# Optimization experiments

Hardware: AMD Instinct MI355X
Metric: run time of the kernel (lower is better)

The kernel has to match this reference:

```python
import jax, jax.numpy as jnp
import numpy as np

D_MODEL = 256
D_INNER = 512   # expand=2
D_STATE = 16
DT_RANK = 16    # ceil(d_model/16)
D_CONV = 4
N_LAYERS = 2    # per direction
B, N = 2, 1024


def _mamba_layer(x, W_in, cw, cb, W_x, W_dt, b_dt, A_log, Dp, W_out):
    """One mamba_ssm.Mamba forward. x: (B, L, d_model)."""
    Bb, L, _ = x.shape
    xz = x @ W_in.T                        # (B, L, 2*d_inner)
    di = xz.shape[-1] // 2
    xc, z = xz[..., :di], xz[..., di:]
    # causal depthwise conv1d, kernel D_CONV, left-pad d_conv-1
    K = cw.shape[-1]
    xp = jnp.pad(xc, ((0, 0), (K - 1, 0), (0, 0)))
    xc = sum(xp[:, k:k + L, :] * cw[:, k] for k in range(K)) + cb
    xc = jax.nn.silu(xc)
    # input-dependent dt, B, C
    dbl = xc @ W_x.T                       # (B, L, dt_rank + 2*d_state)
    ds = A_log.shape[-1]
    dt = dbl[..., :DT_RANK]
    Bm = dbl[..., DT_RANK:DT_RANK + ds]    # (B, L, d_state)
    Cm = dbl[..., DT_RANK + ds:]           # (B, L, d_state)
    dt = jax.nn.softplus(dt @ W_dt.T + b_dt)  # (B, L, d_inner)
    A = -jnp.exp(A_log)                    # (d_inner, d_state)
    dA = jnp.exp(dt[..., None] * A)                          # (B, L, di, ds)
    dBx = dt[..., None] * Bm[:, :, None, :] * xc[..., None]  # (B, L, di, ds)

    def step(h, inp):
        a_t, b_t, c_t = inp                # (B,di,ds),(B,di,ds),(B,ds)
        h = a_t * h + b_t
        y_t = jnp.einsum('bds,bs->bd', h, c_t)
        return h, y_t

    h0 = jnp.zeros((Bb, di, ds), x.dtype)
    _, ys = jax.lax.scan(step, h0, (dA.transpose(1, 0, 2, 3),
                                    dBx.transpose(1, 0, 2, 3),
                                    Cm.transpose(1, 0, 2)))
    y = ys.transpose(1, 0, 2) + xc * Dp    # skip term D*x
    y = y * jax.nn.silu(z)                 # gate
    return y @ W_out.T                     # (B, L, d_model)


def setup_inputs() -> dict:
    key = jax.random.key(0)
    ks = jax.random.split(key, 10)
    s = 0.05  # weight scale for numerical stability
    nlay = 2 * N_LAYERS  # forward layers then backward layers
    return {
        "x": jax.random.normal(ks[0], (B, N, D_MODEL), jnp.float32),
        "in_proj": jax.random.normal(ks[1], (nlay, 2 * D_INNER, D_MODEL), jnp.float32) * s,
        "conv_w": jax.random.normal(ks[2], (nlay, D_INNER, D_CONV), jnp.float32) * s,
        "conv_b": jax.random.normal(ks[3], (nlay, D_INNER), jnp.float32) * s,
        "x_proj": jax.random.normal(ks[4], (nlay, DT_RANK + 2 * D_STATE, D_INNER), jnp.float32) * s,
        "dt_proj": jax.random.normal(ks[5], (nlay, D_INNER, DT_RANK), jnp.float32) * s,
        "dt_bias": jax.random.normal(ks[6], (nlay, D_INNER), jnp.float32) * s,
        "A_log": jax.random.uniform(ks[7], (nlay, D_INNER, D_STATE), jnp.float32),
        "D": jax.random.uniform(ks[8], (nlay, D_INNER), jnp.float32),
        "out_proj": jax.random.normal(ks[9], (nlay, D_MODEL, D_INNER), jnp.float32) * s,
    }


def reference(x, in_proj, conv_w, conv_b, x_proj, dt_proj, dt_bias, A_log, D, out_proj):
    n = in_proj.shape[0] // 2
    x_fwd = x
    for i in range(n):
        x_fwd = _mamba_layer(x_fwd, in_proj[i], conv_w[i], conv_b[i], x_proj[i],
                             dt_proj[i], dt_bias[i], A_log[i], D[i], out_proj[i])
    x_bwd = x[:, ::-1, :]
    for i in range(n, 2 * n):
        x_bwd = _mamba_layer(x_bwd, in_proj[i], conv_w[i], conv_b[i], x_proj[i],
                             dt_proj[i], dt_bias[i], A_log[i], D[i], out_proj[i])
    x_bwd = x_bwd[:, ::-1, :]
    return jnp.concatenate([x_fwd, x_bwd], axis=-1)  # (B, N, 2*d_model)
```

## Files before the change

kernel.cpp:

```cpp
#include <hip/hip_runtime.h>
#include <math.h>

#define G 2
#define BB 2
#define L 1024
#define DM 256
#define DI 512
#define DS 16
#define DR 16
#define CH 64
#define CL 16
#define RTOT (G*BB*L)
#define YSTR 520
#define XSTR 520

#define NWIN  (4 * 2 * DI * DM)
#define NWOUT (4 * DM * DI)
#define NWX   (4 * 48 * DI)

typedef short bh8 __attribute__((ext_vector_type(8)));
typedef float f4x __attribute__((ext_vector_type(4)));

__device__ __forceinline__ float silu_f(float x) { return x / (1.f + __expf(-x)); }
__device__ __forceinline__ float softplus_f(float x) {
    return (x > 20.f) ? x : __logf(1.f + __expf(x));
}

__device__ __forceinline__ unsigned short f2bf(float f) {
    unsigned u = __float_as_uint(f);
    unsigned r = u + 0x7FFFu + ((u >> 16) & 1u);
    return (unsigned short)(r >> 16);
}
__device__ __forceinline__ float bf2f(unsigned short s) {
    return __uint_as_float(((unsigned)s) << 16);
}

__global__ __launch_bounds__(256) void cvtW3(
    const float* __restrict__ Wa, short* __restrict__ Wah, short* __restrict__ Wal, int n4a,
    const float* __restrict__ Wb, short* __restrict__ Wbh, short* __restrict__ Wbl, int n4b,
    const float* __restrict__ Wc, short* __restrict__ Wch, short* __restrict__ Wcl, int n4c)
{
    int i = blockIdx.x * 256 + threadIdx.x;
    const float* W; short *Wh, *Wl;
    if (i < n4a) { W = Wa; Wh = Wah; Wl = Wal; }
    else if (i < n4a + n4b) { i -= n4a; W = Wb; Wh = Wbh; Wl = Wbl; }
    else if (i < n4a + n4b + n4c) { i -= n4a + n4b; W = Wc; Wh = Wch; Wl = Wcl; }
    else return;
    float4 v = *(const float4*)&W[(size_t)i * 4];
    short4 h, l;
    unsigned short s;
    s = f2bf(v.x); h.x = (short)s; l.x = (short)f2bf(v.x - bf2f(s));
    s = f2bf(v.y); h.y = (short)s; l.y = (short)f2bf(v.y - bf2f(s));
    s = f2bf(v.z); h.z = (short)s; l.z = (short)f2bf(v.z - bf2f(s));
    s = f2bf(v.w); h.w = (short)s; l.w = (short)f2bf(v.w - bf2f(s));
    *(short4*)&Wh[(size_t)i * 4] = h;
    *(short4*)&Wl[(size_t)i * 4] = l;
}

template<int AMAP>
__global__ __launch_bounds__(256) void mfma_inproj(
    const float* __restrict__ Ax,
    const short* __restrict__ Ah, const short* __restrict__ Al,
    const short* __restrict__ Wh, const short* __restrict__ Wl,
    int step, float* __restrict__ C)
{
    constexpr int BM = 128, Ktot = DM, Nout = 2 * DI, ldc = 1024;
    __shared__ short As_hi[BM * 40];
    __shared__ short As_lo[BM * 40];
    __shared__ short Bs_hi[64 * 40];
    __shared__ short Bs_lo[64 * 40];

    const int row0 = blockIdx.y * BM;
    const int col0 = blockIdx.x * 64;
    const int g    = row0 >> 11;
    const int lay  = g * 2 + step;
    const short* Whg = Wh + (size_t)lay * Nout * Ktot;
    const short* Wlg = Wl + (size_t)lay * Nout * Ktot;
    const int t    = threadIdx.x;
    const int lane = t & 63, wv = t >> 6;
    const int m = lane & 15, quad = lane >> 4;
    const int wr = wv >> 1, wc = wv & 1;
    const int NT = Ktot / 32;

    float4 pa[4];
    short4 pah[4], pal[4], pbh[2], pbl[2];
    auto loadT = [&](int kt) {
        const int kb = kt * 32;
        #pragma unroll
        for (int i = 0; i < 4; i++) {
            int id = t + 256 * i;
            int row = id >> 3, kq = id & 7;
            if (AMAP == 1) {
                int gr = row0 + row;
                int gg = gr >> 11, b = (gr >> 10) & 1, l = gr & 1023;
                int sl = gg ? (1023 - l) : l;
                pa[i] = *(const float4*)&Ax[(size_t)(b * 1024 + sl) * Ktot + kb + kq * 4];
            } else {
                size_t o = (size_t)(row0 + row) * Ktot + kb + kq * 4;
                pah[i] = *(const short4*)&Ah[o];
                pal[i] = *(const short4*)&Al[o];
            }
        }
        #pragma unroll
        for (int i = 0; i < 2; i++) {
            int id = t + 256 * i;
            int row = id >> 3, kq = id & 7;
            size_t o = (size_t)(col0 + row) * Ktot + kb + kq * 4;
            pbh[i] = *(const short4*)&Whg[o];
            pbl[i] = *(const short4*)&Wlg[o];
        }
    };

    f4x acc[4][2] = {};
    loadT(0);

    for (int kt = 0; kt < NT; kt++) {
        #pragma unroll
        for (int i = 0; i < 4; i++) {
            int id = t + 256 * i;
            int row = id >> 3, kq = id & 7;
            if (AMAP == 1) {
                float4 v = pa[i];
                short4 h, l;
                unsigned short s;
                s = f2bf(v.x); h.x = (short)s; l.x = (short)f2bf(v.x - bf2f(s));
                s = f2bf(v.y); h.y = (short)s; l.y = (short)f2bf(v.y - bf2f(s));
                s = f2bf(v.z); h.z = (short)s; l.z = (short)f2bf(v.z - bf2f(s));
                s = f2bf(v.w); h.w = (short)s; l.w = (short)f2bf(v.w - bf2f(s));
                *(short4*)&As_hi[row * 40 + kq * 4] = h;
                *(short4*)&As_lo[row * 40 + kq * 4] = l;
            } else {
                *(short4*)&As_hi[row * 40 + kq * 4] = pah[i];
                *(short4*)&As_lo[row * 40 + kq * 4] = pal[i];
            }
        }
        #pragma unroll
        for (int i = 0; i < 2; i++) {
            int id = t + 256 * i;
            int row = id >> 3, kq = id & 7;
            *(short4*)&Bs_hi[row * 40 + kq * 4] = pbh[i];
            *(short4*)&Bs_lo[row * 40 + kq * 4] = pbl[i];
        }
        __syncthreads();
        if (kt + 1 < NT) loadT(kt + 1);

        bh8 ah[4], al[4], bh[2], bl[2];
        #pragma unroll
        for (int p = 0; p < 4; p++) {
            int r = wr * 64 + p * 16 + m;
            ah[p] = *(bh8*)&As_hi[r * 40 + quad * 8];
            al[p] = *(bh8*)&As_lo[r * 40 + quad * 8];
        }
        #pragma unroll
        for (int q = 0; q < 2; q++) {
            int r = wc * 32 + q * 16 + m;
            bh[q] = *(bh8*)&Bs_hi[r * 40 + quad * 8];
            bl[q] = *(bh8*)&Bs_lo[r * 40 + quad * 8];
        }
        #pragma unroll
        for (int p = 0; p < 4; p++)
            #pragma unroll
            for (int q = 0; q < 2; q++) {
                acc[p][q] = __builtin_amdgcn_mfma_f32_16x16x32_bf16(ah[p], bh[q], acc[p][q], 0, 0, 0);
                acc[p][q] = __builtin_amdgcn_mfma_f32_16x16x32_bf16(ah[p], bl[q], acc[p][q], 0, 0, 0);
                acc[p][q] = __builtin_amdgcn_mfma_f32_16x16x32_bf16(al[p], bh[q], acc[p][q], 0, 0, 0);
            }
        __syncthreads();
    }

    #pragma unroll
    for (int p = 0; p < 4; p++)
        #pragma unroll
        for (int q = 0; q < 2; q++) {
            int gcol = col0 + wc * 32 + q * 16 + m;
            #pragma unroll
            for (int r = 0; r < 4; r++) {
                int grow = row0 + wr * 64 + p * 16 + quad * 4 + r;
                C[(size_t)grow * ldc + gcol] = acc[p][q][r];
            }
        }
}

__global__ __launch_bounds__(512) void scanA2(
    const float* __restrict__ XZ, const float* __restrict__ cw,
    const float* __restrict__ cb,
    const short* __restrict__ Wxh, const short* __restrict__ Wxl,
    const float* __restrict__ A_log, const float* __restrict__ Wdt,
    const float* __restrict__ bdt,
    float* __restrict__ XCb, float* __restrict__ DBLc,
    float* __restrict__ Aprod, float* __restrict__ Hend, int step)
{
    __shared__ short xcH[CL * XSTR];
    __shared__ short xcL[CL * XSTR];
    __shared__ float part[8][CL][48];
    __shared__ float dbl[CL][48];

    const int blk = blockIdx.x;
    const int c  = blk & (CH - 1);
    const int gb = blk >> 6;
    const int g  = gb >> 1;
    const int lay = g * 2 + step;
    const int d  = threadIdx.x;
    const int r0 = gb * L + c * CL;

    float4 w4 = *(const float4*)&cw[((size_t)lay * DI + d) * 4];
    float cbv = cb[(size_t)lay * DI + d];
    float xz[CL + 3];
    #pragma unroll
    for (int j = 0; j < CL + 3; j++) {
        int lr = c * CL + j - 3;
        xz[j] = (lr < 0) ? 0.f : XZ[(size_t)(gb * L + lr) * 1024 + d];
    }
    float xc[CL];
    #pragma unroll
    for (int tt = 0; tt < CL; tt++) {
        float v = cbv + w4.x * xz[tt] + w4.y * xz[tt + 1]
                      + w4.z * xz[tt + 2] + w4.w * xz[tt + 3];
        v = silu_f(v);
        xc[tt] = v;
        XCb[(size_t)(r0 + tt) * DI + d] = v;
        unsigned short hs = f2bf(v);
        xcH[tt * XSTR + d] = (short)hs;
        xcL[tt * XSTR + d] = (short)f2bf(v - bf2f(hs));
    }
    __syncthreads();

    {
        const int lane = d & 63, wv = d >> 6;
        const int m = lane & 15, quad = lane >> 4;
        const int ks = wv * 64;
        const size_t wb = (size_t)lay * 48 * DI;
        f4x acc[3] = {};
        #pragma unroll
        for (int kt = 0; kt < 2; kt++) {
            const int kb = ks + kt * 32 + quad * 8;
            bh8 ah = *(bh8*)&xcH[m * XSTR + kb];
            bh8 al = *(bh8*)&xcL[m * XSTR + kb];
            #pragma unroll
            for (int f = 0; f < 3; f++) {
                bh8 bh = *(const bh8*)&Wxh[wb + (size_t)(f * 16 + m) * DI + kb];
                bh8 bl = *(const bh8*)&Wxl[wb + (size_t)(f * 16 + m) * DI + kb];
                acc[f] = __builtin_amdgcn_mfma_f32_16x16x32_bf16(ah, bh, acc[f], 0, 0, 0);
                acc[f] = __builtin_amdgcn_mfma_f32_16x16x32_bf16(ah, bl, acc[f], 0, 0, 0);
                acc[f] = __builtin_amdgcn_mfma_f32_16x16x32_bf16(al, bh, acc[f], 0, 0, 0);
            }
        }
        #pragma unroll
        for (int f = 0; f < 3; f++)
            #pragma unroll
            for (int r = 0; r < 4; r++)
                part[wv][quad * 4 + r][f * 16 + m] = acc[f][r];
    }
    __syncthreads();

    for (int o = d; o < CL * 48; o += 512) {
        int tt = o / 48, cc = o - tt * 48;
        float v = 0.f;
        #pragma unroll
        for (int w = 0; w < 8; w++) v += part[w][tt][cc];
        dbl[tt][cc] = v;
        DBLc[(size_t)(r0 + tt) * 48 + cc] = v;
    }

    float wdt[16];
    const float* wrow = Wdt + ((size_t)lay * DI + d) * DR;
    #pragma unroll
    for (int k = 0; k < 16; k += 4) {
        float4 v = *(const float4*)&wrow[k];
        wdt[k] = v.x; wdt[k + 1] = v.y; wdt[k + 2] = v.z; wdt[k + 3] = v.w;
    }
    float bias = bdt[(size_t)lay * DI + d];

    float a[DS], h[DS], ap[DS];
    const float* al = A_log + ((size_t)lay * DI + d) * DS;
    #pragma unroll
    for (int s = 0; s < DS; s++) { a[s] = -__expf(al[s]); h[s] = 0.f; ap[s] = 1.f; }
    __syncthreads();

    for (int tt = 0; tt < CL; tt++) {
        float dtr = bias;
        #pragma unroll
        for (int k = 0; k < 16; k++) dtr += dbl[tt][k] * wdt[k];
        float dt = softplus_f(dtr);
        float dx = dt * xc[tt];
        #pragma unroll
        for (int s = 0; s < DS; s++) {
            float da = __expf(dt * a[s]);
            h[s] = da * h[s] + dx * dbl[tt][16 + s];
            ap[s] *= da;
        }
    }
    size_t base = ((size_t)(gb * DI + d) * CH + c) * DS;
    #pragma unroll
    for (int q = 0; q < 4; q++) {
        *(float4*)&Aprod[base + q * 4] = make_float4(ap[q*4], ap[q*4+1], ap[q*4+2], ap[q*4+3]);
        *(float4*)&Hend [base + q * 4] = make_float4(h[q*4],  h[q*4+1],  h[q*4+2],  h[q*4+3]);
    }
}

__global__ __launch_bounds__(256) void scanCombine(
    const float* __restrict__ Aprod, const float* __restrict__ Hend,
    float* __restrict__ Hinit)
{
    int idx = blockIdx.x * 256 + threadIdx.x;
    int s  = idx & 15;
    int gd = idx >> 4;
    size_t base = (size_t)gd * CH * DS + s;
    float h = 0.f;
    for (int c0 = 0; c0 < CH; c0 += 8) {
        float ap[8], e[8];
        #pragma unroll
        for (int j = 0; j < 8; j++) {
            size_t o = base + (size_t)(c0 + j) * DS;
            ap[j] = Aprod[o]; e[j] = Hend[o];
        }
        #pragma unroll
        for (int j = 0; j < 8; j++) {
            Hinit[base + (size_t)(c0 + j) * DS] = h;
            h = ap[j] * h + e[j];
        }
    }
}

template<int OUTMODE>
__global__ __launch_bounds__(512) void scanB_fused(
    const float* __restrict__ XCb, const float* __restrict__ DBLc,
    const float* __restrict__ XZ, const float* __restrict__ A_log,
    const float* __restrict__ Wdt, const float* __restrict__ bdt,
    const float* __restrict__ Dp, const float* __restrict__ Hinit,
    const short* __restrict__ Woh, const short* __restrict__ Wol,
    float* __restrict__ Cout, short* __restrict__ Ph, short* __restrict__ Pl,
    int step)
{
    __shared__ float dbl[CL][48];
    __shared__ short Ys_hi[CL * YSTR];
    __shared__ short Ys_lo[CL * YSTR];
    int blk = blockIdx.x;
    int c  = blk & (CH - 1);
    int gb = blk >> 6;
    int g  = gb >> 1;
    int lay = g * 2 + step;
    int d = threadIdx.x;
    int r0 = gb * L + c * CL;

    for (int id = threadIdx.x; id < CL * 48; id += 512) {
        int rr = id / 48, cc = id - rr * 48;
        dbl[rr][cc] = DBLc[(size_t)(r0 + rr) * 48 + cc];
    }

    float xc[CL], zz[CL];
    #pragma unroll
    for (int tt = 0; tt < CL; tt++) xc[tt] = XCb[(size_t)(r0 + tt) * DI + d];
    #pragma unroll
    for (int tt = 0; tt < CL; tt++) zz[tt] = XZ[(size_t)(r0 + tt) * 1024 + 512 + d];

    float wdt[16];
    const float* wrow = Wdt + ((size_t)lay * DI + d) * DR;
    #pragma unroll
    for (int k = 0; k < 16; k += 4) {
        float4 v = *(const float4*)&wrow[k];
        wdt[k] = v.x; wdt[k + 1] = v.y; wdt[k + 2] = v.z; wdt[k + 3] = v.w;
    }
    float bias = bdt[(size_t)lay * DI + d];

    float a[DS], h[DS];
    const float* al = A_log + ((size_t)lay * DI + d) * DS;
    size_t base = ((size_t)(gb * DI + d) * CH + c) * DS;
    #pragma unroll
    for (int q = 0; q < 4; q++) {
        float4 hv = *(const float4*)&Hinit[base + q * 4];
        h[q*4] = hv.x; h[q*4+1] = hv.y; h[q*4+2] = hv.z; h[q*4+3] = hv.w;
    }
    #pragma unroll
    for (int s = 0; s < DS; s++) a[s] = -__expf(al[s]);
    float Dv = Dp[(size_t)lay * DI + d];
    __syncthreads();

    #pragma unroll
    for (int tt = 0; tt < CL; tt++) {
        float dtr = bias;
        #pragma unroll
        for (int k = 0; k < 16; k++) dtr += dbl[tt][k] * wdt[k];
        float dt = softplus_f(dtr);
        float dx = dt * xc[tt];
        float y = 0.f;
        #pragma unroll
        for (int s = 0; s < DS; s++) {
            float da = __expf(dt * a[s]);
            h[s] = da * h[s] + dx * dbl[tt][16 + s];
            y += h[s] * dbl[tt][32 + s];
        }
        y += xc[tt] * Dv;
        y *= silu_f(zz[tt]);
        unsigned short hs = f2bf(y);
        Ys_hi[tt * YSTR + d] = (short)hs;
        Ys_lo[tt * YSTR + d] = (short)f2bf(y - bf2f(hs));
    }
    __syncthreads();

    const int lane = threadIdx.x & 63, wv = threadIdx.x >> 6;
    const int m = lane & 15, quad = lane >> 4;
    const size_t wbase = (size_t)lay * DM * DI;

    #pragma unroll
    for (int q = 0; q < 2; q++) {
        const int coln = wv * 32 + q * 16 + m;
        const size_t wrow2 = wbase + (size_t)coln * DI;
        bh8 wh[16], wl[16];
        #pragma unroll
        for (int i = 0; i < 16; i++) {
            const int kk = i * 32 + quad * 8;
            wh[i] = *(const bh8*)&Woh[wrow2 + kk];
            wl[i] = *(const bh8*)&Wol[wrow2 + kk];
        }
        f4x acc = {};
        #pragma unroll
        for (int i = 0; i < 16; i++) {
            const int kk = i * 32 + quad * 8;
            bh8 ahv = *(bh8*)&Ys_hi[m * YSTR + kk];
            bh8 alv = *(bh8*)&Ys_lo[m * YSTR + kk];
            acc = __builtin_amdgcn_mfma_f32_16x16x32_bf16(ahv, wh[i], acc, 0, 0, 0);
            acc = __builtin_amdgcn_mfma_f32_16x16x32_bf16(ahv, wl[i], acc, 0, 0, 0);
            acc = __builtin_amdgcn_mfma_f32_16x16x32_bf16(alv, wh[i], acc, 0, 0, 0);
        }
        #pragma unroll
        for (int r = 0; r < 4; r++) {
            int tt = quad * 4 + r;
            int grow = r0 + tt;
            if (OUTMODE == 0) {
                size_t o = (size_t)grow * DM + coln;
                unsigned short hs = f2bf(acc[r]);
                Ph[o] = (short)hs;
                Pl[o] = (short)f2bf(acc[r] - bf2f(hs));
            } else {
                int b = (grow >> 10) & 1, l = grow & 1023;
                size_t dst = (g == 0)
                    ? ((size_t)(b * 1024 + l) * 512 + coln)
                    : ((size_t)(b * 1024 + (1023 - l)) * 512 + 256 + coln);
                Cout[dst] = acc[r];
            }
        }
    }
}

extern "C" void kernel_launch(void* const* d_in, const int* in_sizes, int n_in,
                              void* d_out, int out_size, void* d_ws, size_t ws_size,
                              hipStream_t stream)
{
    const float* x        = (const float*)d_in[0];
    const float* in_proj  = (const float*)d_in[1];
    const float* conv_w   = (const float*)d_in[2];
    const float* conv_b   = (const float*)d_in[3];
    const float* x_proj   = (const float*)d_in[4];
    const float* dt_proj  = (const float*)d_in[5];
    const float* dt_bias  = (const float*)d_in[6];
    const float* A_log    = (const float*)d_in[7];
    const float* Dp       = (const float*)d_in[8];
    const float* out_proj = (const float*)d_in[9];
    float* out = (float*)d_out;

    float* w = (float*)d_ws;
    size_t o = 0;
    float* XZ    = w + o; o += (size_t)RTOT * 1024;
    float* XCb   = w + o; o += (size_t)RTOT * DI;
    float* Pdbl  = w + o; o += (size_t)8 * RTOT * 48;
    float* DBLc  = w + o; o += (size_t)RTOT * 48;
    float* Aprod = w + o; o += (size_t)G * BB * DI * CH * DS;
    float* Hend  = w + o; o += (size_t)G * BB * DI * CH * DS;
    float* Hinit = w + o; o += (size_t)G * BB * DI * CH * DS;
    short* Wih   = (short*)(w + o); o += NWIN / 2;
    short* Wil   = (short*)(w + o); o += NWIN / 2;
    short* Woh   = (short*)(w + o); o += NWOUT / 2;
    short* Wol   = (short*)(w + o); o += NWOUT / 2;
    short* Ph    = (short*)(w + o); o += (size_t)RTOT * DM / 2;
    short* Pl    = (short*)(w + o); o += (size_t)RTOT * DM / 2;
    short* Wxh   = (short*)Pdbl;
    short* Wxl   = Wxh + NWX;
    (void)ws_size; (void)in_sizes; (void)n_in; (void)out_size;

    {
        int n4a = NWIN / 4, n4b = NWOUT / 4, n4c = NWX / 4;
        cvtW3<<<(n4a + n4b + n4c + 255) / 256, 256, 0, stream>>>(
            in_proj, Wih, Wil, n4a, out_proj, Woh, Wol, n4b,
            x_proj, Wxh, Wxl, n4c);
    }

    for (int step = 0; step < 2; step++) {
        if (step == 0)
            mfma_inproj<1><<<dim3(16, 32), 256, 0, stream>>>(
                x, nullptr, nullptr, Wih, Wil, 0, XZ);
        else
            mfma_inproj<0><<<dim3(16, 32), 256, 0, stream>>>(
                nullptr, Ph, Pl, Wih, Wil, 1, XZ);

        scanA2<<<G * BB * CH, 512, 0, stream>>>(
            XZ, conv_w, conv_b, Wxh, Wxl, A_log, dt_proj, dt_bias,
            XCb, DBLc, Aprod, Hend, step);

        scanCombine<<<(G * BB * DI * DS) / 256, 256, 0, stream>>>(Aprod, Hend, Hinit);

        if (step == 0)
            scanB_fused<0><<<G * BB * CH, 512, 0, stream>>>(
                XCb, DBLc, XZ, A_log, dt_proj, dt_bias, Dp, Hinit,
                Woh, Wol, nullptr, Ph, Pl, 0);
        else
            scanB_fused<1><<<G * BB * CH, 512, 0, stream>>>(
                XCb, DBLc, XZ, A_log, dt_proj, dt_bias, Dp, Hinit,
                Woh, Wol, out, nullptr, nullptr, 1);
    }
}
```

Baseline: 223.6 us.

## Fuse in_proj GEMM into scan-A kernel and split weights on the fly

Removes the separate in_proj GEMM kernel and fuses it into the per-chunk scan kernel. Each 16-row chunk block recomputes its own xz tile, including a 3-row halo for the causal conv, and keeps the conv input in shared memory, writing only z to global. The weight pre-conversion kernel is dropped: in_proj, x_proj and out_proj are read as fp32 and split into bf16 hi/lo pairs inside the MFMA loops. This saves two launches and the full XZ round trip through global memory. In exchange each block redoes weight loads and splits, the halo rows add extra GEMM work, and the in_proj GEMM now runs with a small M tile that gets little weight reuse.

```diff
diff --git a/kernel.cpp b/kernel.cpp
--- a/kernel.cpp
+++ b/kernel.cpp
@@ -14,12 +14,10 @@
 #define YSTR 520
 #define XSTR 520
 
-#define NWIN  (4 * 2 * DI * DM)
-#define NWOUT (4 * DM * DI)
-#define NWX   (4 * 48 * DI)
-
 typedef short bh8 __attribute__((ext_vector_type(8)));
 typedef float f4x __attribute__((ext_vector_type(4)));
+
+#define MFMA16 __builtin_amdgcn_mfma_f32_16x16x32_bf16
 
 __device__ __forceinline__ float silu_f(float x) { return x / (1.f + __expf(-x)); }
 __device__ __forceinline__ float softplus_f(float x) {
@@ -34,188 +32,142 @@
 __device__ __forceinline__ float bf2f(unsigned short s) {
     return __uint_as_float(((unsigned)s) << 16);
 }
-
-__global__ __launch_bounds__(256) void cvtW3(
-    const float* __restrict__ Wa, short* __restrict__ Wah, short* __restrict__ Wal, int n4a,
-    const float* __restrict__ Wb, short* __restrict__ Wbh, short* __restrict__ Wbl, int n4b,
-    const float* __restrict__ Wc, short* __restrict__ Wch, short* __restrict__ Wcl, int n4c)
-{
-    int i = blockIdx.x * 256 + threadIdx.x;
-    const float* W; short *Wh, *Wl;
-    if (i < n4a) { W = Wa; Wh = Wah; Wl = Wal; }
-    else if (i < n4a + n4b) { i -= n4a; W = Wb; Wh = Wbh; Wl = Wbl; }
-    else if (i < n4a + n4b + n4c) { i -= n4a + n4b; W = Wc; Wh = Wch; Wl = Wcl; }
-    else return;
-    float4 v = *(const float4*)&W[(size_t)i * 4];
-    short4 h, l;
+__device__ __forceinline__ void split4s(float4 v, short4& h, short4& l) {
     unsigned short s;
     s = f2bf(v.x); h.x = (short)s; l.x = (short)f2bf(v.x - bf2f(s));
     s = f2bf(v.y); h.y = (short)s; l.y = (short)f2bf(v.y - bf2f(s));
     s = f2bf(v.z); h.z = (short)s; l.z = (short)f2bf(v.z - bf2f(s));
     s = f2bf(v.w); h.w = (short)s; l.w = (short)f2bf(v.w - bf2f(s));
-    *(short4*)&Wh[(size_t)i * 4] = h;
-    *(short4*)&Wl[(size_t)i * 4] = l;
+}
+__device__ __forceinline__ void split8(float4 v0, float4 v1, bh8& h, bh8& l) {
+    float f[8] = {v0.x, v0.y, v0.z, v0.w, v1.x, v1.y, v1.z, v1.w};
+    #pragma unroll
+    for (int j = 0; j < 8; j++) {
+        unsigned short s = f2bf(f[j]);
+        h[j] = (short)s;
+        l[j] = (short)f2bf(f[j] - bf2f(s));
+    }
 }
 
 template<int AMAP>
-__global__ __launch_bounds__(256) void mfma_inproj(
+__global__ __launch_bounds__(512) void megaA(
     const float* __restrict__ Ax,
-    const short* __restrict__ Ah, const short* __restrict__ Al,
-    const short* __restrict__ Wh, const short* __restrict__ Wl,
-    int step, float* __restrict__ C)
-{
-    constexpr int BM = 128, Ktot = DM, Nout = 2 * DI, ldc = 1024;
-    __shared__ short As_hi[BM * 40];
-    __shared__ short As_lo[BM * 40];
-    __shared__ short Bs_hi[64 * 40];
-    __shared__ short Bs_lo[64 * 40];
-
-    const int row0 = blockIdx.y * BM;
-    const int col0 = blockIdx.x * 64;
-    const int g    = row0 >> 11;
-    const int lay  = g * 2 + step;
-    const short* Whg = Wh + (size_t)lay * Nout * Ktot;
-    const short* Wlg = Wl + (size_t)lay * Nout * Ktot;
-    const int t    = threadIdx.x;
-    const int lane = t & 63, wv = t >> 6;
-    const int m = lane & 15, quad = lane >> 4;
-    const int wr = wv >> 1, wc = wv & 1;
-    const int NT = Ktot / 32;
-
-    float4 pa[4];
-    short4 pah[4], pal[4], pbh[2], pbl[2];
-    auto loadT = [&](int kt) {
-        const int kb = kt * 32;
-        #pragma unroll
-        for (int i = 0; i < 4; i++) {
-            int id = t + 256 * i;
-            int row = id >> 3, kq = id & 7;
-            if (AMAP == 1) {
-                int gr = row0 + row;
-                int gg = gr >> 11, b = (gr >> 10) & 1, l = gr & 1023;
-                int sl = gg ? (1023 - l) : l;
-                pa[i] = *(const float4*)&Ax[(size_t)(b * 1024 + sl) * Ktot + kb + kq * 4];
-            } else {
-                size_t o = (size_t)(row0 + row) * Ktot + kb + kq * 4;
-                pah[i] = *(const short4*)&Ah[o];
-                pal[i] = *(const short4*)&Al[o];
-            }
-        }
-        #pragma unroll
-        for (int i = 0; i < 2; i++) {
-            int id = t + 256 * i;
-            int row = id >> 3, kq = id & 7;
-            size_t o = (size_t)(col0 + row) * Ktot + kb + kq * 4;
-            pbh[i] = *(const short4*)&Whg[o];
-            pbl[i] = *(const short4*)&Wlg[o];
-        }
-    };
-
-    f4x acc[4][2] = {};
-    loadT(0);
-
-    for (int kt = 0; kt < NT; kt++) {
-        #pragma unroll
-        for (int i = 0; i < 4; i++) {
-            int id = t + 256 * i;
-            int row = id >> 3, kq = id & 7;
-            if (AMAP == 1) {
-                float4 v = pa[i];
-                short4 h, l;
-                unsigned short s;
-                s = f2bf(v.x); h.x = (short)s; l.x = (short)f2bf(v.x - bf2f(s));
-                s = f2bf(v.y); h.y = (short)s; l.y = (short)f2bf(v.y - bf2f(s));
-                s = f2bf(v.z); h.z = (short)s; l.z = (short)f2bf(v.z - bf2f(s));
-                s = f2bf(v.w); h.w = (short)s; l.w = (short)f2bf(v.w - bf2f(s));
-                *(short4*)&As_hi[row * 40 + kq * 4] = h;
-                *(short4*)&As_lo[row * 40 + kq * 4] = l;
-            } else {
-                *(short4*)&As_hi[row * 40 + kq * 4] = pah[i];
-                *(short4*)&As_lo[row * 40 + kq * 4] = pal[i];
-            }
-        }
-        #pragma unroll
-        for (int i = 0; i < 2; i++) {
-            int id = t + 256 * i;
-            int row = id >> 3, kq = id & 7;
-            *(short4*)&Bs_hi[row * 40 + kq * 4] = pbh[i];
-            *(short4*)&Bs_lo[row * 40 + kq * 4] = pbl[i];
-        }
-        __syncthreads();
-        if (kt + 1 < NT) loadT(kt + 1);
-
-        bh8 ah[4], al[4], bh[2], bl[2];
-        #pragma unroll
-        for (int p = 0; p < 4; p++) {
-            int r = wr * 64 + p * 16 + m;
-            ah[p] = *(bh8*)&As_hi[r * 40 + quad * 8];
-            al[p] = *(bh8*)&As_lo[r * 40 + quad * 8];
-        }
-        #pragma unroll
-        for (int q = 0; q < 2; q++) {
-            int r = wc * 32 + q * 16 + m;
-            bh[q] = *(bh8*)&Bs_hi[r * 40 + quad * 8];
-            bl[q] = *(bh8*)&Bs_lo[r * 40 + quad * 8];
-        }
-        #pragma unroll
-        for (int p = 0; p < 4; p++)
-            #pragma unroll
-            for (int q = 0; q < 2; q++) {
-                acc[p][q] = __builtin_amdgcn_mfma_f32_16x16x32_bf16(ah[p], bh[q], acc[p][q], 0, 0, 0);
-                acc[p][q] = __builtin_amdgcn_mfma_f32_16x16x32_bf16(ah[p], bl[q], acc[p][q], 0, 0, 0);
-                acc[p][q] = __builtin_amdgcn_mfma_f32_16x16x32_bf16(al[p], bh[q], acc[p][q], 0, 0, 0);
-            }
-        __syncthreads();
-    }
-
-    #pragma unroll
-    for (int p = 0; p < 4; p++)
-        #pragma unroll
-        for (int q = 0; q < 2; q++) {
-            int gcol = col0 + wc * 32 + q * 16 + m;
-            #pragma unroll
-            for (int r = 0; r < 4; r++) {
-                int grow = row0 + wr * 64 + p * 16 + quad * 4 + r;
-                C[(size_t)grow * ldc + gcol] = acc[p][q][r];
-            }
-        }
-}
-
-__global__ __launch_bounds__(512) void scanA2(
-    const float* __restrict__ XZ, const float* __restrict__ cw,
-    const float* __restrict__ cb,
-    const short* __restrict__ Wxh, const short* __restrict__ Wxl,
+    const short* __restrict__ APh, const short* __restrict__ APl,
+    const float* __restrict__ Win, const float* __restrict__ cw,
+    const float* __restrict__ cb, const float* __restrict__ Wx,
     const float* __restrict__ A_log, const float* __restrict__ Wdt,
     const float* __restrict__ bdt,
-    float* __restrict__ XCb, float* __restrict__ DBLc,
+    float* __restrict__ XCb, float* __restrict__ Zb, float* __restrict__ DBLc,
     float* __restrict__ Aprod, float* __restrict__ Hend, int step)
 {
-    __shared__ short xcH[CL * XSTR];
-    __shared__ short xcL[CL * XSTR];
-    __shared__ float part[8][CL][48];
-    __shared__ float dbl[CL][48];
+    __shared__ __align__(16) char smem[73008];
+    short* Ah  = (short*)smem;
+    short* Al  = (short*)(smem + 16896);
+    float* xz  = (float*)(smem + 33792);
+    short* xcH = (short*)smem;
+    short* xcL = (short*)(smem + 16640);
+    float* part = (float*)(smem + 33792);
+    float* dbl  = (float*)(smem + 58368);
 
     const int blk = blockIdx.x;
-    const int c  = blk & (CH - 1);
-    const int gb = blk >> 6;
-    const int g  = gb >> 1;
+    const int c   = blk & (CH - 1);
+    const int gb  = blk >> 6;
+    const int g   = gb >> 1;
     const int lay = g * 2 + step;
-    const int d  = threadIdx.x;
-    const int r0 = gb * L + c * CL;
-
+    const int tid = threadIdx.x;
+    const int r0  = gb * L + c * CL;
+    const int lane = tid & 63, wv = tid >> 6;
+    const int m = lane & 15, quad = lane >> 4;
+
+    #pragma unroll
+    for (int i = 0; i < 4; i++) {
+        int id = tid + 512 * i;
+        int row = id >> 6, kq = id & 63;
+        int gr  = r0 - 16 + row;
+        int grc = (gr < gb * L) ? gb * L : gr;
+        if (AMAP == 1) {
+            int b = (grc >> 10) & 1, l = grc & 1023;
+            int sl = g ? (1023 - l) : l;
+            float4 v = *(const float4*)&Ax[(size_t)(b * 1024 + sl) * DM + kq * 4];
+            short4 h4, l4; split4s(v, h4, l4);
+            *(short4*)&Ah[row * 264 + kq * 4] = h4;
+            *(short4*)&Al[row * 264 + kq * 4] = l4;
+        } else {
+            size_t o = (size_t)grc * DM + kq * 4;
+            *(short4*)&Ah[row * 264 + kq * 4] = *(const short4*)&APh[o];
+            *(short4*)&Al[row * 264 + kq * 4] = *(const short4*)&APl[o];
+        }
+    }
+    __syncthreads();
+
+    const float* Wg = Win + (size_t)lay * 1024 * DM;
+    #pragma unroll
+    for (int ct = 0; ct < 2; ct++) {
+        const int colb = ct * 512 + wv * 64;
+        const int mt0 = ct;
+        f4x acc[2][4] = {};
+        for (int kt = 0; kt < 8; kt++) {
+            const int kb = kt * 32 + quad * 8;
+            bh8 ahf[2], alf[2];
+            #pragma unroll
+            for (int mt = 0; mt < 2; mt++) {
+                if (mt < mt0) continue;
+                ahf[mt] = *(bh8*)&Ah[(mt * 16 + m) * 264 + kb];
+                alf[mt] = *(bh8*)&Al[(mt * 16 + m) * 264 + kb];
+            }
+            float4 braw[4][2];
+            #pragma unroll
+            for (int nt = 0; nt < 4; nt++) {
+                const float* bp = &Wg[(size_t)(colb + nt * 16 + m) * DM + kb];
+                braw[nt][0] = *(const float4*)bp;
+                braw[nt][1] = *(const float4*)(bp + 4);
+            }
+            #pragma unroll
+            for (int nt = 0; nt < 4; nt++) {
+                bh8 bh, bl; split8(braw[nt][0], braw[nt][1], bh, bl);
+                #pragma unroll
+                for (int mt = 0; mt < 2; mt++) {
+                    if (mt < mt0) continue;
+                    acc[mt][nt] = MFMA16(ahf[mt], bh, acc[mt][nt], 0, 0, 0);
+                    acc[mt][nt] = MFMA16(ahf[mt], bl, acc[mt][nt], 0, 0, 0);
+                    acc[mt][nt] = MFMA16(alf[mt], bh, acc[mt][nt], 0, 0, 0);
+                }
+            }
+        }
+        #pragma unroll
+        for (int nt = 0; nt < 4; nt++) {
+            int gcol = colb + nt * 16 + m;
+            #pragma unroll
+            for (int mt = 0; mt < 2; mt++) {
+                if (mt < mt0) continue;
+                #pragma unroll
+                for (int r = 0; r < 4; r++) {
+                    int i = mt * 16 + quad * 4 + r;
+                    float v = acc[mt][nt][r];
+                    if (ct == 0) {
+                        if (i >= 13) xz[(i - 13) * 516 + gcol] = v;
+                    } else {
+                        if (i >= 16)
+                            Zb[(size_t)(r0 + i - 16) * 512 + (gcol - 512)] = v;
+                    }
+                }
+            }
+        }
+    }
+    __syncthreads();
+
+    const int d = tid;
     float4 w4 = *(const float4*)&cw[((size_t)lay * DI + d) * 4];
     float cbv = cb[(size_t)lay * DI + d];
-    float xz[CL + 3];
-    #pragma unroll
-    for (int j = 0; j < CL + 3; j++) {
-        int lr = c * CL + j - 3;
-        xz[j] = (lr < 0) ? 0.f : XZ[(size_t)(gb * L + lr) * 1024 + d];
-    }
+    float xzv[CL + 3];
+    #pragma unroll
+    for (int j = 0; j < CL + 3; j++)
+        xzv[j] = (c * CL + j - 3 < 0) ? 0.f : xz[j * 516 + d];
     float xc[CL];
     #pragma unroll
     for (int tt = 0; tt < CL; tt++) {
-        float v = cbv + w4.x * xz[tt] + w4.y * xz[tt + 1]
-                      + w4.z * xz[tt + 2] + w4.w * xz[tt + 3];
+        float v = cbv + w4.x * xzv[tt] + w4.y * xzv[tt + 1]
+                      + w4.z * xzv[tt + 2] + w4.w * xzv[tt + 3];
         v = silu_f(v);
         xc[tt] = v;
         XCb[(size_t)(r0 + tt) * DI + d] = v;
@@ -226,11 +178,9 @@
     __syncthreads();
 
     {
-        const int lane = d & 63, wv = d >> 6;
-        const int m = lane & 15, quad = lane >> 4;
         const int ks = wv * 64;
-        const size_t wb = (size_t)lay * 48 * DI;
-        f4x acc[3] = {};
+        const float* Wxg = Wx + (size_t)lay * 48 * DI;
+        f4x acc3[3] = {};
         #pragma unroll
         for (int kt = 0; kt < 2; kt++) {
             const int kb = ks + kt * 32 + quad * 8;
@@ -238,18 +188,19 @@
             bh8 al = *(bh8*)&xcL[m * XSTR + kb];
             #pragma unroll
             for (int f = 0; f < 3; f++) {
-                bh8 bh = *(const bh8*)&Wxh[wb + (size_t)(f * 16 + m) * DI + kb];
-                bh8 bl = *(const bh8*)&Wxl[wb + (size_t)(f * 16 + m) * DI + kb];
-                acc[f] = __builtin_amdgcn_mfma_f32_16x16x32_bf16(ah, bh, acc[f], 0, 0, 0);
-                acc[f] = __builtin_amdgcn_mfma_f32_16x16x32_bf16(ah, bl, acc[f], 0, 0, 0);
-                acc[f] = __builtin_amdgcn_mfma_f32_16x16x32_bf16(al, bh, acc[f], 0, 0, 0);
+                const float* wp = &Wxg[(size_t)(f * 16 + m) * DI + kb];
+                bh8 bh, bl;
+                split8(*(const float4*)wp, *(const float4*)(wp + 4), bh, bl);
+                acc3[f] = MFMA16(ah, bh, acc3[f], 0, 0, 0);
+                acc3[f] = MFMA16(ah, bl, acc3[f], 0, 0, 0);
+                acc3[f] = MFMA16(al, bh, acc3[f], 0, 0, 0);
             }
         }
         #pragma unroll
         for (int f = 0; f < 3; f++)
             #pragma unroll
             for (int r = 0; r < 4; r++)
-                part[wv][quad * 4 + r][f * 16 + m] = acc[f][r];
+                part[(wv * 16 + quad * 4 + r) * 48 + f * 16 + m] = acc3[f][r];
     }
     __syncthreads();
 
@@ -257,8 +208,8 @@
         int tt = o / 48, cc = o - tt * 48;
         float v = 0.f;
         #pragma unroll
-        for (int w = 0; w < 8; w++) v += part[w][tt][cc];
-        dbl[tt][cc] = v;
+        for (int w = 0; w < 8; w++) v += part[(w * 16 + tt) * 48 + cc];
+        dbl[tt * 48 + cc] = v;
         DBLc[(size_t)(r0 + tt) * 48 + cc] = v;
     }
 
@@ -280,13 +231,13 @@
     for (int tt = 0; tt < CL; tt++) {
         float dtr = bias;
         #pragma unroll
-        for (int k = 0; k < 16; k++) dtr += dbl[tt][k] * wdt[k];
+        for (int k = 0; k < 16; k++) dtr += dbl[tt * 48 + k] * wdt[k];
         float dt = softplus_f(dtr);
         float dx = dt * xc[tt];
         #pragma unroll
         for (int s = 0; s < DS; s++) {
             float da = __expf(dt * a[s]);
-            h[s] = da * h[s] + dx * dbl[tt][16 + s];
+            h[s] = da * h[s] + dx * dbl[tt * 48 + 16 + s];
             ap[s] *= da;
         }
     }
@@ -325,10 +276,10 @@
 template<int OUTMODE>
 __global__ __launch_bounds__(512) void scanB_fused(
     const float* __restrict__ XCb, const float* __restrict__ DBLc,
-    const float* __restrict__ XZ, const float* __restrict__ A_log,
+    const float* __restrict__ Zb, const float* __restrict__ A_log,
     const float* __restrict__ Wdt, const float* __restrict__ bdt,
     const float* __restrict__ Dp, const float* __restrict__ Hinit,
-    const short* __restrict__ Woh, const short* __restrict__ Wol,
+    const float* __restrict__ Wout,
     float* __restrict__ Cout, short* __restrict__ Ph, short* __restrict__ Pl,
     int step)
 {
@@ -352,7 +303,7 @@
     #pragma unroll
     for (int tt = 0; tt < CL; tt++) xc[tt] = XCb[(size_t)(r0 + tt) * DI + d];
     #pragma unroll
-    for (int tt = 0; tt < CL; tt++) zz[tt] = XZ[(size_t)(r0 + tt) * 1024 + 512 + d];
+    for (int tt = 0; tt < CL; tt++) zz[tt] = Zb[(size_t)(r0 + tt) * 512 + d];
 
     float wdt[16];
     const float* wrow = Wdt + ((size_t)lay * DI + d) * DR;
@@ -400,18 +351,17 @@
 
     const int lane = threadIdx.x & 63, wv = threadIdx.x >> 6;
     const int m = lane & 15, quad = lane >> 4;
-    const size_t wbase = (size_t)lay * DM * DI;
+    const float* Wog = Wout + (size_t)lay * DM * DI;
 
     #pragma unroll
     for (int q = 0; q < 2; q++) {
         const int coln = wv * 32 + q * 16 + m;
-        const size_t wrow2 = wbase + (size_t)coln * DI;
+        const float* wrp = &Wog[(size_t)coln * DI];
         bh8 wh[16], wl[16];
         #pragma unroll
         for (int i = 0; i < 16; i++) {
-            const int kk = i * 32 + quad * 8;
-            wh[i] = *(const bh8*)&Woh[wrow2 + kk];
-            wl[i] = *(const bh8*)&Wol[wrow2 + kk];
+            const float* p = wrp + i * 32 + quad * 8;
+            split8(*(const float4*)p, *(const float4*)(p + 4), wh[i], wl[i]);
         }
         f4x acc = {};
         #pragma unroll
@@ -419,9 +369,9 @@
             const int kk = i * 32 + quad * 8;
             bh8 ahv = *(bh8*)&Ys_hi[m * YSTR + kk];
             bh8 alv = *(bh8*)&Ys_lo[m * YSTR + kk];
-            acc = __builtin_amdgcn_mfma_f32_16x16x32_bf16(ahv, wh[i], acc, 0, 0, 0);
-            acc = __builtin_amdgcn_mfma_f32_16x16x32_bf16(ahv, wl[i], acc, 0, 0, 0);
-            acc = __builtin_amdgcn_mfma_f32_16x16x32_bf16(alv, wh[i], acc, 0, 0, 0);
+            acc = MFMA16(ahv, wh[i], acc, 0, 0, 0);
+            acc = MFMA16(ahv, wl[i], acc, 0, 0, 0);
+            acc = MFMA16(alv, wh[i], acc, 0, 0, 0);
         }
         #pragma unroll
         for (int r = 0; r < 4; r++) {
@@ -461,51 +411,35 @@
 
     float* w = (float*)d_ws;
     size_t o = 0;
-    float* XZ    = w + o; o += (size_t)RTOT * 1024;
     float* XCb   = w + o; o += (size_t)RTOT * DI;
-    float* Pdbl  = w + o; o += (size_t)8 * RTOT * 48;
+    float* Zb    = w + o; o += (size_t)RTOT * 512;
     float* DBLc  = w + o; o += (size_t)RTOT * 48;
     float* Aprod = w + o; o += (size_t)G * BB * DI * CH * DS;
     float* Hend  = w + o; o += (size_t)G * BB * DI * CH * DS;
     float* Hinit = w + o; o += (size_t)G * BB * DI * CH * DS;
-    short* Wih   = (short*)(w + o); o += NWIN / 2;
-    short* Wil   = (short*)(w + o); o += NWIN / 2;
-    short* Woh   = (short*)(w + o); o += NWOUT / 2;
-    short* Wol   = (short*)(w + o); o += NWOUT / 2;
     short* Ph    = (short*)(w + o); o += (size_t)RTOT * DM / 2;
     short* Pl    = (short*)(w + o); o += (size_t)RTOT * DM / 2;
-    short* Wxh   = (short*)Pdbl;
-    short* Wxl   = Wxh + NWX;
     (void)ws_size; (void)in_sizes; (void)n_in; (void)out_size;
-
-    {
-        int n4a = NWIN / 4, n4b = NWOUT / 4, n4c = NWX / 4;
-        cvtW3<<<(n4a + n4b + n4c + 255) / 256, 256, 0, stream>>>(
-            in_proj, Wih, Wil, n4a, out_proj, Woh, Wol, n4b,
-            x_proj, Wxh, Wxl, n4c);
-    }
 
     for (int step = 0; step < 2; step++) {
         if (step == 0)
-            mfma_inproj<1><<<dim3(16, 32), 256, 0, stream>>>(
-                x, nullptr, nullptr, Wih, Wil, 0, XZ);
+            megaA<1><<<G * BB * CH, 512, 0, stream>>>(
+                x, nullptr, nullptr, in_proj, conv_w, conv_b, x_proj,
+                A_log, dt_proj, dt_bias, XCb, Zb, DBLc, Aprod, Hend, 0);
         else
-            mfma_inproj<0><<<dim3(16, 32), 256, 0, stream>>>(
-                nullptr, Ph, Pl, Wih, Wil, 1, XZ);
-
-        scanA2<<<G * BB * CH, 512, 0, stream>>>(
-            XZ, conv_w, conv_b, Wxh, Wxl, A_log, dt_proj, dt_bias,
-            XCb, DBLc, Aprod, Hend, step);
+            megaA<0><<<G * BB * CH, 512, 0, stream>>>(
+                nullptr, Ph, Pl, in_proj, conv_w, conv_b, x_proj,
+                A_log, dt_proj, dt_bias, XCb, Zb, DBLc, Aprod, Hend, 1);
 
         scanCombine<<<(G * BB * DI * DS) / 256, 256, 0, stream>>>(Aprod, Hend, Hinit);
 
         if (step == 0)
             scanB_fused<0><<<G * BB * CH, 512, 0, stream>>>(
-                XCb, DBLc, XZ, A_log, dt_proj, dt_bias, Dp, Hinit,
-                Woh, Wol, nullptr, Ph, Pl, 0);
+                XCb, DBLc, Zb, A_log, dt_proj, dt_bias, Dp, Hinit,
+                out_proj, nullptr, Ph, Pl, 0);
         else
             scanB_fused<1><<<G * BB * CH, 512, 0, stream>>>(
-                XCb, DBLc, XZ, A_log, dt_proj, dt_bias, Dp, Hinit,
-                Woh, Wol, out, nullptr, nullptr, 1);
-    }
-}
+                XCb, DBLc, Zb, A_log, dt_proj, dt_bias, Dp, Hinit,
+                out_proj, out, nullptr, nullptr, 1);
+    }
+}
```

New measurement: 254.1 us. 1.14x slower.

## Fold weight bf16 splitting into GEMMs, recompute conv in scanB, widen inproj tile

Applied to the files above, without the earlier changes.

Removes the separate weight-conversion kernel. The in_proj, x_proj and out_proj GEMMs now read fp32 weights and split them into bf16 hi/lo on the fly. The XCb buffer write and read are dropped by recomputing the causal conv plus SiLU inside scanB_fused from XZ. The in_proj tile grows to 128x128, which halves the grid and raises reuse. This trades one launch and some global traffic for extra per-block conversion ALU work, since out_proj weights are re-split in every block, and for lower in_proj occupancy.

```diff
diff --git a/kernel.cpp b/kernel.cpp
--- a/kernel.cpp
+++ b/kernel.cpp
@@ -14,12 +14,10 @@
 #define YSTR 520
 #define XSTR 520
 
-#define NWIN  (4 * 2 * DI * DM)
-#define NWOUT (4 * DM * DI)
-#define NWX   (4 * 48 * DI)
-
 typedef short bh8 __attribute__((ext_vector_type(8)));
 typedef float f4x __attribute__((ext_vector_type(4)));
+
+#define MFMA16 __builtin_amdgcn_mfma_f32_16x16x32_bf16
 
 __device__ __forceinline__ float silu_f(float x) { return x / (1.f + __expf(-x)); }
 __device__ __forceinline__ float softplus_f(float x) {
@@ -34,48 +32,41 @@
 __device__ __forceinline__ float bf2f(unsigned short s) {
     return __uint_as_float(((unsigned)s) << 16);
 }
-
-__global__ __launch_bounds__(256) void cvtW3(
-    const float* __restrict__ Wa, short* __restrict__ Wah, short* __restrict__ Wal, int n4a,
-    const float* __restrict__ Wb, short* __restrict__ Wbh, short* __restrict__ Wbl, int n4b,
-    const float* __restrict__ Wc, short* __restrict__ Wch, short* __restrict__ Wcl, int n4c)
-{
-    int i = blockIdx.x * 256 + threadIdx.x;
-    const float* W; short *Wh, *Wl;
-    if (i < n4a) { W = Wa; Wh = Wah; Wl = Wal; }
-    else if (i < n4a + n4b) { i -= n4a; W = Wb; Wh = Wbh; Wl = Wbl; }
-    else if (i < n4a + n4b + n4c) { i -= n4a + n4b; W = Wc; Wh = Wch; Wl = Wcl; }
-    else return;
-    float4 v = *(const float4*)&W[(size_t)i * 4];
-    short4 h, l;
+__device__ __forceinline__ void split4s(float4 v, short4& h, short4& l) {
     unsigned short s;
     s = f2bf(v.x); h.x = (short)s; l.x = (short)f2bf(v.x - bf2f(s));
     s = f2bf(v.y); h.y = (short)s; l.y = (short)f2bf(v.y - bf2f(s));
     s = f2bf(v.z); h.z = (short)s; l.z = (short)f2bf(v.z - bf2f(s));
     s = f2bf(v.w); h.w = (short)s; l.w = (short)f2bf(v.w - bf2f(s));
-    *(short4*)&Wh[(size_t)i * 4] = h;
-    *(short4*)&Wl[(size_t)i * 4] = l;
+}
+__device__ __forceinline__ void split8(float4 v0, float4 v1, bh8& h, bh8& l) {
+    float f[8] = {v0.x, v0.y, v0.z, v0.w, v1.x, v1.y, v1.z, v1.w};
+    #pragma unroll
+    for (int j = 0; j < 8; j++) {
+        unsigned short s = f2bf(f[j]);
+        h[j] = (short)s;
+        l[j] = (short)f2bf(f[j] - bf2f(s));
+    }
 }
 
 template<int AMAP>
 __global__ __launch_bounds__(256) void mfma_inproj(
     const float* __restrict__ Ax,
-    const short* __restrict__ Ah, const short* __restrict__ Al,
-    const short* __restrict__ Wh, const short* __restrict__ Wl,
+    const short* __restrict__ APh, const short* __restrict__ APl,
+    const float* __restrict__ Win,
     int step, float* __restrict__ C)
 {
-    constexpr int BM = 128, Ktot = DM, Nout = 2 * DI, ldc = 1024;
-    __shared__ short As_hi[BM * 40];
-    __shared__ short As_lo[BM * 40];
-    __shared__ short Bs_hi[64 * 40];
-    __shared__ short Bs_lo[64 * 40];
-
-    const int row0 = blockIdx.y * BM;
-    const int col0 = blockIdx.x * 64;
+    constexpr int Ktot = DM, ldc = 1024;
+    __shared__ short As_hi[128 * 40];
+    __shared__ short As_lo[128 * 40];
+    __shared__ short Bs_hi[128 * 40];
+    __shared__ short Bs_lo[128 * 40];
+
+    const int row0 = blockIdx.y * 128;
+    const int col0 = blockIdx.x * 128;
     const int g    = row0 >> 11;
     const int lay  = g * 2 + step;
-    const short* Whg = Wh + (size_t)lay * Nout * Ktot;
-    const short* Wlg = Wl + (size_t)lay * Nout * Ktot;
+    const float* Wg = Win + (size_t)lay * 1024 * Ktot;
     const int t    = threadIdx.x;
     const int lane = t & 63, wv = t >> 6;
     const int m = lane & 15, quad = lane >> 4;
@@ -83,7 +74,8 @@
     const int NT = Ktot / 32;
 
     float4 pa[4];
-    short4 pah[4], pal[4], pbh[2], pbl[2];
+    short4 pah[4], pal[4];
+    float4 pb[4];
     auto loadT = [&](int kt) {
         const int kb = kt * 32;
         #pragma unroll
@@ -97,21 +89,14 @@
                 pa[i] = *(const float4*)&Ax[(size_t)(b * 1024 + sl) * Ktot + kb + kq * 4];
             } else {
                 size_t o = (size_t)(row0 + row) * Ktot + kb + kq * 4;
-                pah[i] = *(const short4*)&Ah[o];
-                pal[i] = *(const short4*)&Al[o];
-            }
-        }
-        #pragma unroll
-        for (int i = 0; i < 2; i++) {
-            int id = t + 256 * i;
-            int row = id >> 3, kq = id & 7;
-            size_t o = (size_t)(col0 + row) * Ktot + kb + kq * 4;
-            pbh[i] = *(const short4*)&Whg[o];
-            pbl[i] = *(const short4*)&Wlg[o];
+                pah[i] = *(const short4*)&APh[o];
+                pal[i] = *(const short4*)&APl[o];
+            }
+            pb[i] = *(const float4*)&Wg[(size_t)(col0 + row) * Ktot + kb + kq * 4];
         }
     };
 
-    f4x acc[4][2] = {};
+    f4x acc[4][4] = {};
     loadT(0);
 
     for (int kt = 0; kt < NT; kt++) {
@@ -120,31 +105,21 @@
             int id = t + 256 * i;
             int row = id >> 3, kq = id & 7;
             if (AMAP == 1) {
-                float4 v = pa[i];
-                short4 h, l;
-                unsigned short s;
-                s = f2bf(v.x); h.x = (short)s; l.x = (short)f2bf(v.x - bf2f(s));
-                s = f2bf(v.y); h.y = (short)s; l.y = (short)f2bf(v.y - bf2f(s));
-                s = f2bf(v.z); h.z = (short)s; l.z = (short)f2bf(v.z - bf2f(s));
-                s = f2bf(v.w); h.w = (short)s; l.w = (short)f2bf(v.w - bf2f(s));
-                *(short4*)&As_hi[row * 40 + kq * 4] = h;
-                *(short4*)&As_lo[row * 40 + kq * 4] = l;
+                short4 h4, l4; split4s(pa[i], h4, l4);
+                *(short4*)&As_hi[row * 40 + kq * 4] = h4;
+                *(short4*)&As_lo[row * 40 + kq * 4] = l4;
             } else {
                 *(short4*)&As_hi[row * 40 + kq * 4] = pah[i];
                 *(short4*)&As_lo[row * 40 + kq * 4] = pal[i];
             }
-        }
-        #pragma unroll
-        for (int i = 0; i < 2; i++) {
-            int id = t + 256 * i;
-            int row = id >> 3, kq = id & 7;
-            *(short4*)&Bs_hi[row * 40 + kq * 4] = pbh[i];
-            *(short4*)&Bs_lo[row * 40 + kq * 4] = pbl[i];
+            short4 h4, l4; split4s(pb[i], h4, l4);
+            *(short4*)&Bs_hi[row * 40 + kq * 4] = h4;
+            *(short4*)&Bs_lo[row * 40 + kq * 4] = l4;
         }
         __syncthreads();
         if (kt + 1 < NT) loadT(kt + 1);
 
-        bh8 ah[4], al[4], bh[2], bl[2];
+        bh8 ah[4], al[4], bh[4], bl[4];
         #pragma unroll
         for (int p = 0; p < 4; p++) {
             int r = wr * 64 + p * 16 + m;
@@ -152,18 +127,18 @@
             al[p] = *(bh8*)&As_lo[r * 40 + quad * 8];
         }
         #pragma unroll
-        for (int q = 0; q < 2; q++) {
-            int r = wc * 32 + q * 16 + m;
+        for (int q = 0; q < 4; q++) {
+            int r = wc * 64 + q * 16 + m;
             bh[q] = *(bh8*)&Bs_hi[r * 40 + quad * 8];
             bl[q] = *(bh8*)&Bs_lo[r * 40 + quad * 8];
         }
         #pragma unroll
         for (int p = 0; p < 4; p++)
             #pragma unroll
-            for (int q = 0; q < 2; q++) {
-                acc[p][q] = __builtin_amdgcn_mfma_f32_16x16x32_bf16(ah[p], bh[q], acc[p][q], 0, 0, 0);
-                acc[p][q] = __builtin_amdgcn_mfma_f32_16x16x32_bf16(ah[p], bl[q], acc[p][q], 0, 0, 0);
-                acc[p][q] = __builtin_amdgcn_mfma_f32_16x16x32_bf16(al[p], bh[q], acc[p][q], 0, 0, 0);
+            for (int q = 0; q < 4; q++) {
+                acc[p][q] = MFMA16(ah[p], bh[q], acc[p][q], 0, 0, 0);
+                acc[p][q] = MFMA16(ah[p], bl[q], acc[p][q], 0, 0, 0);
+                acc[p][q] = MFMA16(al[p], bh[q], acc[p][q], 0, 0, 0);
             }
         __syncthreads();
     }
@@ -171,8 +146,8 @@
     #pragma unroll
     for (int p = 0; p < 4; p++)
         #pragma unroll
-        for (int q = 0; q < 2; q++) {
-            int gcol = col0 + wc * 32 + q * 16 + m;
+        for (int q = 0; q < 4; q++) {
+            int gcol = col0 + wc * 64 + q * 16 + m;
             #pragma unroll
             for (int r = 0; r < 4; r++) {
                 int grow = row0 + wr * 64 + p * 16 + quad * 4 + r;
@@ -183,11 +158,10 @@
 
 __global__ __launch_bounds__(512) void scanA2(
     const float* __restrict__ XZ, const float* __restrict__ cw,
-    const float* __restrict__ cb,
-    const short* __restrict__ Wxh, const short* __restrict__ Wxl,
+    const float* __restrict__ cb, const float* __restrict__ Wx,
     const float* __restrict__ A_log, const float* __restrict__ Wdt,
     const float* __restrict__ bdt,
-    float* __restrict__ XCb, float* __restrict__ DBLc,
+    float* __restrict__ DBLc,
     float* __restrict__ Aprod, float* __restrict__ Hend, int step)
 {
     __shared__ short xcH[CL * XSTR];
@@ -218,7 +192,6 @@
                       + w4.z * xz[tt + 2] + w4.w * xz[tt + 3];
         v = silu_f(v);
         xc[tt] = v;
-        XCb[(size_t)(r0 + tt) * DI + d] = v;
         unsigned short hs = f2bf(v);
         xcH[tt * XSTR + d] = (short)hs;
         xcL[tt * XSTR + d] = (short)f2bf(v - bf2f(hs));
@@ -229,8 +202,8 @@
         const int lane = d & 63, wv = d >> 6;
         const int m = lane & 15, quad = lane >> 4;
         const int ks = wv * 64;
-        const size_t wb = (size_t)lay * 48 * DI;
-        f4x acc[3] = {};
+        const float* Wxg = Wx + (size_t)lay * 48 * DI;
+        f4x acc3[3] = {};
         #pragma unroll
         for (int kt = 0; kt < 2; kt++) {
             const int kb = ks + kt * 32 + quad * 8;
@@ -238,18 +211,19 @@
             bh8 al = *(bh8*)&xcL[m * XSTR + kb];
             #pragma unroll
             for (int f = 0; f < 3; f++) {
-                bh8 bh = *(const bh8*)&Wxh[wb + (size_t)(f * 16 + m) * DI + kb];
-                bh8 bl = *(const bh8*)&Wxl[wb + (size_t)(f * 16 + m) * DI + kb];
-                acc[f] = __builtin_amdgcn_mfma_f32_16x16x32_bf16(ah, bh, acc[f], 0, 0, 0);
-                acc[f] = __builtin_amdgcn_mfma_f32_16x16x32_bf16(ah, bl, acc[f], 0, 0, 0);
-                acc[f] = __builtin_amdgcn_mfma_f32_16x16x32_bf16(al, bh, acc[f], 0, 0, 0);
+                const float* wp = &Wxg[(size_t)(f * 16 + m) * DI + kb];
+                bh8 bh, bl;
+                split8(*(const float4*)wp, *(const float4*)(wp + 4), bh, bl);
+                acc3[f] = MFMA16(ah, bh, acc3[f], 0, 0, 0);
+                acc3[f] = MFMA16(ah, bl, acc3[f], 0, 0, 0);
+                acc3[f] = MFMA16(al, bh, acc3[f], 0, 0, 0);
             }
         }
         #pragma unroll
         for (int f = 0; f < 3; f++)
             #pragma unroll
             for (int r = 0; r < 4; r++)
-                part[wv][quad * 4 + r][f * 16 + m] = acc[f][r];
+                part[wv][quad * 4 + r][f * 16 + m] = acc3[f][r];
     }
     __syncthreads();
 
@@ -324,11 +298,12 @@
 
 template<int OUTMODE>
 __global__ __launch_bounds__(512) void scanB_fused(
-    const float* __restrict__ XCb, const float* __restrict__ DBLc,
-    const float* __restrict__ XZ, const float* __restrict__ A_log,
+    const float* __restrict__ XZ, const float* __restrict__ DBLc,
+    const float* __restrict__ cw, const float* __restrict__ cb,
+    const float* __restrict__ A_log,
     const float* __restrict__ Wdt, const float* __restrict__ bdt,
     const float* __restrict__ Dp, const float* __restrict__ Hinit,
-    const short* __restrict__ Woh, const short* __restrict__ Wol,
+    const float* __restrict__ Wout,
     float* __restrict__ Cout, short* __restrict__ Ph, short* __restrict__ Pl,
     int step)
 {
@@ -348,9 +323,21 @@
         dbl[rr][cc] = DBLc[(size_t)(r0 + rr) * 48 + cc];
     }
 
+    float4 w4 = *(const float4*)&cw[((size_t)lay * DI + d) * 4];
+    float cbv = cb[(size_t)lay * DI + d];
+    float xzv[CL + 3];
+    #pragma unroll
+    for (int j = 0; j < CL + 3; j++) {
+        int lr = c * CL + j - 3;
+        xzv[j] = (lr < 0) ? 0.f : XZ[(size_t)(gb * L + lr) * 1024 + d];
+    }
     float xc[CL], zz[CL];
     #pragma unroll
-    for (int tt = 0; tt < CL; tt++) xc[tt] = XCb[(size_t)(r0 + tt) * DI + d];
+    for (int tt = 0; tt < CL; tt++) {
+        float v = cbv + w4.x * xzv[tt] + w4.y * xzv[tt + 1]
+                      + w4.z * xzv[tt + 2] + w4.w * xzv[tt + 3];
+        xc[tt] = silu_f(v);
+    }
     #pragma unroll
     for (int tt = 0; tt < CL; tt++) zz[tt] = XZ[(size_t)(r0 + tt) * 1024 + 512 + d];
 
@@ -400,18 +387,17 @@
 
     const int lane = threadIdx.x & 63, wv = threadIdx.x >> 6;
     const int m = lane & 15, quad = lane >> 4;
-    const size_t wbase = (size_t)lay * DM * DI;
+    const float* Wog = Wout + (size_t)lay * DM * DI;
 
     #pragma unroll
     for (int q = 0; q < 2; q++) {
         const int coln = wv * 32 + q * 16 + m;
-        const size_t wrow2 = wbase + (size_t)coln * DI;
+        const float* wrp = &Wog[(size_t)coln * DI];
         bh8 wh[16], wl[16];
         #pragma unroll
         for (int i = 0; i < 16; i++) {
-            const int kk = i * 32 + quad * 8;
-            wh[i] = *(const bh8*)&Woh[wrow2 + kk];
-            wl[i] = *(const bh8*)&Wol[wrow2 + kk];
+            const float* p = wrp + i * 32 + quad * 8;
+            split8(*(const float4*)p, *(const float4*)(p + 4), wh[i], wl[i]);
         }
         f4x acc = {};
         #pragma unroll
@@ -419,9 +405,9 @@
             const int kk = i * 32 + quad * 8;
             bh8 ahv = *(bh8*)&Ys_hi[m * YSTR + kk];
             bh8 alv = *(bh8*)&Ys_lo[m * YSTR + kk];
-            acc = __builtin_amdgcn_mfma_f32_16x16x32_bf16(ahv, wh[i], acc, 0, 0, 0);
-            acc = __builtin_amdgcn_mfma_f32_16x16x32_bf16(ahv, wl[i], acc, 0, 0, 0);
-            acc = __builtin_amdgcn_mfma_f32_16x16x32_bf16(alv, wh[i], acc, 0, 0, 0);
+            acc = MFMA16(ahv, wh[i], acc, 0, 0, 0);
+            acc = MFMA16(ahv, wl[i], acc, 0, 0, 0);
+            acc = MFMA16(alv, wh[i], acc, 0, 0, 0);
         }
         #pragma unroll
         for (int r = 0; r < 4; r++) {
@@ -462,50 +448,35 @@
     float* w = (float*)d_ws;
     size_t o = 0;
     float* XZ    = w + o; o += (size_t)RTOT * 1024;
-    float* XCb   = w + o; o += (size_t)RTOT * DI;
-    float* Pdbl  = w + o; o += (size_t)8 * RTOT * 48;
     float* DBLc  = w + o; o += (size_t)RTOT * 48;
     float* Aprod = w + o; o += (size_t)G * BB * DI * CH * DS;
     float* Hend  = w + o; o += (size_t)G * BB * DI * CH * DS;
     float* Hinit = w + o; o += (size_t)G * BB * DI * CH * DS;
-    short* Wih   = (short*)(w + o); o += NWIN / 2;
-    short* Wil   = (short*)(w + o); o += NWIN / 2;
-    short* Woh   = (short*)(w + o); o += NWOUT / 2;
-    short* Wol   = (short*)(w + o); o += NWOUT / 2;
     short* Ph    = (short*)(w + o); o += (size_t)RTOT * DM / 2;
     short* Pl    = (short*)(w + o); o += (size_t)RTOT * DM / 2;
-    short* Wxh   = (short*)Pdbl;
-    short* Wxl   = Wxh + NWX;
     (void)ws_size; (void)in_sizes; (void)n_in; (void)out_size;
-
-    {
-        int n4a = NWIN / 4, n4b = NWOUT / 4, n4c = NWX / 4;
-        cvtW3<<<(n4a + n4b + n4c + 255) / 256, 256, 0, stream>>>(
-            in_proj, Wih, Wil, n4a, out_proj, Woh, Wol, n4b,
-            x_proj, Wxh, Wxl, n4c);
-    }
 
     for (int step = 0; step < 2; step++) {
         if (step == 0)
-            mfma_inproj<1><<<dim3(16, 32), 256, 0, stream>>>(
-                x, nullptr, nullptr, Wih, Wil, 0, XZ);
+            mfma_inproj<1><<<dim3(8, 32), 256, 0, stream>>>(
+                x, nullptr, nullptr, in_proj, 0, XZ);
         else
-            mfma_inproj<0><<<dim3(16, 32), 256, 0, stream>>>(
-                nullptr, Ph, Pl, Wih, Wil, 1, XZ);
+            mfma_inproj<0><<<dim3(8, 32), 256, 0, stream>>>(
+                nullptr, Ph, Pl, in_proj, 1, XZ);
 
         scanA2<<<G * BB * CH, 512, 0, stream>>>(
-            XZ, conv_w, conv_b, Wxh, Wxl, A_log, dt_proj, dt_bias,
-            XCb, DBLc, Aprod, Hend, step);
+            XZ, conv_w, conv_b, x_proj, A_log, dt_proj, dt_bias,
+            DBLc, Aprod, Hend, step);
 
         scanCombine<<<(G * BB * DI * DS) / 256, 256, 0, stream>>>(Aprod, Hend, Hinit);
 
         if (step == 0)
             scanB_fused<0><<<G * BB * CH, 512, 0, stream>>>(
-                XCb, DBLc, XZ, A_log, dt_proj, dt_bias, Dp, Hinit,
-                Woh, Wol, nullptr, Ph, Pl, 0);
+                XZ, DBLc, conv_w, conv_b, A_log, dt_proj, dt_bias, Dp, Hinit,
+                out_proj, nullptr, Ph, Pl, 0);
         else
             scanB_fused<1><<<G * BB * CH, 512, 0, stream>>>(
-                XCb, DBLc, XZ, A_log, dt_proj, dt_bias, Dp, Hinit,
-                Woh, Wol, out, nullptr, nullptr, 1);
-    }
-}
+                XZ, DBLc, conv_w, conv_b, A_log, dt_proj, dt_bias, Dp, Hinit,
+                out_proj, out, nullptr, nullptr, 1);
+    }
+}
```

Measured after the change: 230.8 us. 1.03x slower.
